# Kernel optimization log

Hardware: AMD Instinct MI355X
Metric: run time of the kernel (lower is better)

Reference implementation:

```python
import jax, jax.numpy as jnp
import numpy as np

B, S, D = 4, 2048, 1024
H = 16
HD = D // H  # 64


def setup_inputs() -> dict:
    key = jax.random.key(0)
    ks = jax.random.split(key, 6)
    scale = 1.0 / np.sqrt(D)
    return {
        "x": jax.random.normal(ks[0], (B, S, D), dtype=jnp.float32),
        "Wq": jax.random.normal(ks[1], (D, D), dtype=jnp.float32) * scale,
        "Wk": jax.random.normal(ks[2], (D, D), dtype=jnp.float32) * scale,
        "Wv": jax.random.normal(ks[3], (D, D), dtype=jnp.float32) * scale,
        "Wo": jax.random.normal(ks[4], (D, D), dtype=jnp.float32) * scale,
        "bo": jax.random.normal(ks[5], (D,), dtype=jnp.float32) * scale,
    }


def reference(x, Wq, Wk, Wv, Wo, bo):
    b, s, _ = x.shape
    q = (x @ Wq).reshape(b, s, H, HD)
    k = (x @ Wk).reshape(b, s, H, HD)
    v = (x @ Wv).reshape(b, s, H, HD)
    # scores: [b, h, q, k]
    scores = jnp.einsum("bqhd,bkhd->bhqk", q, k)
    # causal mask (upper triangle, diagonal=1, is masked out)
    causal = jnp.tril(jnp.ones((s, s), dtype=bool))
    scores = jnp.where(causal, scores, -jnp.inf)
    # NOTE: source divides by head_dim**2 (keys.shape[-1]**2), not sqrt(head_dim)
    attn = jax.nn.softmax(scores / (HD ** 2), axis=-1)
    ctx = jnp.einsum("bhqk,bkhd->bqhd", attn, v).reshape(b, s, D)
    return ctx @ Wo + bo
```

## Files before the change

### kernel.cpp

```cpp
#include <hip/hip_runtime.h>
#include <hip/hip_bf16.h>
#include <stdint.h>

typedef short          bf16x8 __attribute__((ext_vector_type(8)));
typedef float          f32x4  __attribute__((ext_vector_type(4)));
typedef float          f32x16 __attribute__((ext_vector_type(16)));
typedef unsigned short u16x8  __attribute__((ext_vector_type(8)));

#define MFMA_BF16(a, b, c) __builtin_amdgcn_mfma_f32_16x16x32_bf16((a), (b), (c), 0, 0, 0)
#define MFMA32(a, b, c)    __builtin_amdgcn_mfma_f32_32x32x16_bf16((a), (b), (c), 0, 0, 0)

__device__ __forceinline__ void gl2lds16(const void* g, void* l) {
  __builtin_amdgcn_global_load_lds((const __attribute__((address_space(1))) void*)g,
                                   (__attribute__((address_space(3))) void*)l,
                                   16, 0, 0);
}

__device__ __forceinline__ unsigned short f2bf(float f) {
  union { float f; unsigned int u; } v;
  v.f = f;
  unsigned int r = v.u + 0x7FFFu + ((v.u >> 16) & 1u);
  return (unsigned short)(r >> 16);
}

__device__ __forceinline__ unsigned int pack2tr(float lo, float hi) {
  union { float f; unsigned int u; } a, b;
  a.f = lo; b.f = hi;
  return __builtin_amdgcn_perm(b.u, a.u, 0x07060302u);
}

__global__ void k_convert_x(const float* __restrict__ x, unsigned short* __restrict__ xb) {
  int i = (blockIdx.x * 256 + threadIdx.x) * 8;
  float4 a = *(const float4*)(x + i);
  float4 b = *(const float4*)(x + i + 4);
  u16x8 o;
  o[0] = f2bf(a.x); o[1] = f2bf(a.y); o[2] = f2bf(a.z); o[3] = f2bf(a.w);
  o[4] = f2bf(b.x); o[5] = f2bf(b.y); o[6] = f2bf(b.z); o[7] = f2bf(b.w);
  *(u16x8*)(xb + i) = o;
}

__global__ void k_transpose_w(const float* __restrict__ W0, const float* __restrict__ W1,
                              const float* __restrict__ W2, const float* __restrict__ W3,
                              unsigned short* __restrict__ T0, unsigned short* __restrict__ T1,
                              unsigned short* __restrict__ T2, unsigned short* __restrict__ T3) {
  const float* W = (blockIdx.z == 0) ? W0 : (blockIdx.z == 1) ? W1 : (blockIdx.z == 2) ? W2 : W3;
  unsigned short* T = (blockIdx.z == 0) ? T0 : (blockIdx.z == 1) ? T1 : (blockIdx.z == 2) ? T2 : T3;
  __shared__ float tile[32][33];
  int n0 = blockIdx.x * 32, k0 = blockIdx.y * 32;
  int tx = threadIdx.x & 31, ty = threadIdx.x >> 5;
#pragma unroll
  for (int i = 0; i < 4; ++i)
    tile[ty + i * 8][tx] = W[(size_t)(k0 + ty + i * 8) * 1024 + n0 + tx];
  __syncthreads();
#pragma unroll
  for (int i = 0; i < 4; ++i)
    T[(size_t)(n0 + ty + i * 8) * 1024 + k0 + tx] = f2bf(tile[tx][ty + i * 8]);
}

__global__ void k_transpose_v(const unsigned short* __restrict__ V, unsigned short* __restrict__ Vt) {
  int bh = blockIdx.y;
  int b = bh >> 4, h = bh & 15;
  int s0 = blockIdx.x * 64;
  __shared__ unsigned short t[64][72];
  int rowh = threadIdx.x >> 3, cg = threadIdx.x & 7;
#pragma unroll
  for (int i = 0; i < 2; ++i) {
    int s = rowh + i * 32;
    *(u16x8*)&t[s][cg * 8] =
        *(const u16x8*)(V + (size_t)(b * 2048 + s0 + s) * 1024 + h * 64 + cg * 8);
  }
  __syncthreads();
#pragma unroll
  for (int i = 0; i < 2; ++i) {
    int d = rowh + i * 32;
    u16x8 v;
#pragma unroll
    for (int j = 0; j < 8; ++j) v[j] = t[cg * 8 + j][d];
    *(u16x8*)(Vt + (size_t)(bh * 64 + d) * 2048 + s0 + cg * 8) = v;
  }
}

template <bool OUT_F32>
__global__ __launch_bounds__(256, 3)
void k_gemm128(const unsigned short* __restrict__ A,
               const unsigned short* __restrict__ Bt0, const unsigned short* __restrict__ Bt1,
               const unsigned short* __restrict__ Bt2,
               void* C0, void* C1, void* C2,
               const float* __restrict__ bias) {
  const int tid = threadIdx.x;
  const int w = tid >> 6, lane = tid & 63;
  const int quad = lane >> 4, t16 = lane & 15;
  const int wm = w >> 1, wn = w & 1;
  const int ysel = blockIdx.y >> 3;
  const unsigned short* Bt = (ysel == 0) ? Bt0 : (ysel == 1) ? Bt1 : Bt2;
  void* Cv = (ysel == 0) ? C0 : (ysel == 1) ? C1 : C2;
  const int m0 = blockIdx.x * 128;
  const int n0 = (blockIdx.y & 7) * 128;

  __shared__ unsigned short As[2][128 * 32];
  __shared__ unsigned short Bs[2][128 * 32];

  f32x4 acc[4][4];
#pragma unroll
  for (int i = 0; i < 4; ++i)
#pragma unroll
    for (int j = 0; j < 4; ++j) acc[i][j] = (f32x4){0.f, 0.f, 0.f, 0.f};

  const int arow0 = w * 32 + (lane >> 2);
  const int arow1 = arow0 + 16;
  const int ac0 = (lane & 3) ^ ((arow0 >> 1) & 3);
  const int ac1 = (lane & 3) ^ ((arow1 >> 1) & 3);
  const unsigned short* Ap0 = A + (size_t)(m0 + arow0) * 1024 + ac0 * 8;
  const unsigned short* Ap1 = A + (size_t)(m0 + arow1) * 1024 + ac1 * 8;
  const unsigned short* Bp0 = Bt + (size_t)(n0 + arow0) * 1024 + ac0 * 8;
  const unsigned short* Bp1 = Bt + (size_t)(n0 + arow1) * 1024 + ac1 * 8;

  auto loadT = [&](int kk) {
    const int bufi = kk & 1;
    const int ko = kk * 32;
    gl2lds16(Ap0 + ko, &As[bufi][w * 1024]);
    gl2lds16(Ap1 + ko, &As[bufi][w * 1024 + 512]);
    gl2lds16(Bp0 + ko, &Bs[bufi][w * 1024]);
    gl2lds16(Bp1 + ko, &Bs[bufi][w * 1024 + 512]);
  };

  const int ga = quad ^ ((t16 >> 1) & 3);
  const int arows = wm * 64 + t16;
  const int brows = wn * 64 + t16;

  loadT(0);
  __syncthreads();

  for (int kk = 0; kk < 32; ++kk) {
    if (kk + 1 < 32) loadT(kk + 1);
    const unsigned short* Asb = As[kk & 1];
    const unsigned short* Bsb = Bs[kk & 1];
    bf16x8 af[4], bfr[4];
#pragma unroll
    for (int mi = 0; mi < 4; ++mi)
      af[mi] = *(const bf16x8*)&Asb[(arows + mi * 16) * 32 + ga * 8];
#pragma unroll
    for (int ni = 0; ni < 4; ++ni)
      bfr[ni] = *(const bf16x8*)&Bsb[(brows + ni * 16) * 32 + ga * 8];
#pragma unroll
    for (int mi = 0; mi < 4; ++mi)
#pragma unroll
      for (int ni = 0; ni < 4; ++ni)
        acc[mi][ni] = MFMA_BF16(af[mi], bfr[ni], acc[mi][ni]);
    __syncthreads();
  }

#pragma unroll
  for (int mi = 0; mi < 4; ++mi) {
    const int row = m0 + wm * 64 + mi * 16 + quad * 4;
#pragma unroll
    for (int ni = 0; ni < 4; ++ni) {
      const int col = n0 + wn * 64 + ni * 16 + t16;
      f32x4 v = acc[mi][ni];
      if (OUT_F32) {
        float* Cf = (float*)Cv;
        const float bv = bias[col];
#pragma unroll
        for (int r = 0; r < 4; ++r) Cf[(size_t)(row + r) * 1024 + col] = v[r] + bv;
      } else {
        unsigned short* Cb = (unsigned short*)Cv;
#pragma unroll
        for (int r = 0; r < 4; ++r) Cb[(size_t)(row + r) * 1024 + col] = f2bf(v[r]);
      }
    }
  }
}

__global__ __launch_bounds__(256, 2)
void k_attn(const unsigned short* __restrict__ Q, const unsigned short* __restrict__ K,
            const unsigned short* __restrict__ Vt, unsigned short* __restrict__ ctx) {
  const int tid = threadIdx.x;
  const int w = tid >> 6, lane = tid & 63;
  const int ln31 = lane & 31, hh = lane >> 5;
  const int bh = blockIdx.x;
  const int qt = 15 - blockIdx.y;
  const int b = bh >> 4, h = bh & 15;
  const int q0 = qt * 128;

  __shared__ unsigned short Ks[2][128 * 64];
  __shared__ unsigned short Vts[2][64 * 128];
  __shared__ unsigned short Ps[4 * 32 * 64];
  unsigned short* Qs = Ps;
  unsigned short* Pw = &Ps[w * 2048];

#pragma unroll
  for (int i = 0; i < 4; ++i) {
    const int chunk = w * 4 + i;
    const int row = chunk * 8 + (lane >> 3);
    const int c = (lane & 7) ^ (row & 7);
    gl2lds16(Q + (size_t)(b * 2048 + q0 + row) * 1024 + h * 64 + c * 8, &Qs[chunk * 512]);
  }

  auto loadKV = [&](int kt) {
    const int k0 = kt * 128;
    const int bufi = kt & 1;
#pragma unroll
    for (int i = 0; i < 4; ++i) {
      const int chunk = w * 4 + i;
      const int row = chunk * 8 + (lane >> 3);
      const int c = (lane & 7) ^ (row & 7);
      gl2lds16(K + (size_t)(b * 2048 + k0 + row) * 1024 + h * 64 + c * 8,
               &Ks[bufi][chunk * 512]);
    }
#pragma unroll
    for (int i = 0; i < 4; ++i) {
      const int chunk = w * 4 + i;
      const int row = chunk * 4 + (lane >> 4);
      const int c = (lane & 15) ^ (row & 7);
      gl2lds16(Vt + (size_t)(bh * 64 + row) * 2048 + k0 + c * 8, &Vts[bufi][chunk * 512]);
    }
  };

  loadKV(0);
  __syncthreads();

  const int qq = ln31;
  bf16x8 qf[4];
#pragma unroll
  for (int t = 0; t < 4; ++t)
    qf[t] = *(const bf16x8*)&Qs[(w * 32 + qq) * 64 + ((2 * t + hh) ^ (qq & 7)) * 8];

  f32x16 kZ;
#pragma unroll
  for (int i = 0; i < 16; ++i) kZ[i] = 0.f;
  f32x16 oacc0 = kZ, oacc1 = kZ, lacc = kZ;
  bf16x8 onesB;
#pragma unroll
  for (int i = 0; i < 8; ++i) onesB[i] = (short)0x3F80;

  const float C1 = 2.44140625e-4f;
  const float C2 = 2.9802322387695312e-8f;

  const unsigned short* KsB = Ks[0];
  const unsigned short* VtsB = Vts[0];

  auto sgroup = [&](int g, bool masked) {
    f32x16 sc;
#pragma unroll
    for (int t = 0; t < 4; ++t) {
      bf16x8 kf = *(const bf16x8*)&KsB[(g * 32 + ln31) * 64 + ((2 * t + hh) ^ (ln31 & 7)) * 8];
      sc = (t == 0) ? MFMA32(kf, qf[0], kZ) : MFMA32(kf, qf[t], sc);
    }
#pragma unroll
    for (int r2 = 0; r2 < 4; ++r2) {
      float ev[4];
#pragma unroll
      for (int r = 0; r < 4; ++r) {
        const float s = sc[r2 * 4 + r];
        float e = fmaf(s, fmaf(s, C2, C1), 1.0f);
        if (masked) {
          const int krow = r + 8 * r2 + 4 * hh;
          if (krow > qq) e = 0.f;
        }
        ev[r] = e;
      }
      uint2 pp;
      pp.x = pack2tr(ev[0], ev[1]);
      pp.y = pack2tr(ev[2], ev[3]);
      *(uint2*)&Pw[qq * 64 + ((((g & 1) * 4 + r2) ^ (qq & 7)) * 8) + hh * 4] = pp;
    }
  };
  auto zgroup = [&](int g) {
    uint2 z; z.x = 0u; z.y = 0u;
#pragma unroll
    for (int r2 = 0; r2 < 4; ++r2)
      *(uint2*)&Pw[qq * 64 + ((((g & 1) * 4 + r2) ^ (qq & 7)) * 8) + hh * 4] = z;
  };
  auto pv = [&](int half) {
#pragma unroll
    for (int t = 0; t < 4; ++t) {
      bf16x8 pf = *(const bf16x8*)&Pw[qq * 64 + ((2 * t + hh) ^ (qq & 7)) * 8];
      lacc = MFMA32(pf, onesB, lacc);
      const int gv = 2 * t + hh + half * 8;
      bf16x8 vf0 = *(const bf16x8*)&VtsB[ln31 * 128 + ((gv ^ (ln31 & 7)) * 8)];
      bf16x8 vf1 = *(const bf16x8*)&VtsB[(32 + ln31) * 128 + ((gv ^ (ln31 & 7)) * 8)];
      oacc0 = MFMA32(pf, vf0, oacc0);
      oacc1 = MFMA32(pf, vf1, oacc1);
    }
  };

  const int nk = qt + 1;
  for (int kt = 0; kt < nk; ++kt) {
    if (kt + 1 < nk) loadKV(kt + 1);
    KsB = Ks[kt & 1];
    VtsB = Vts[kt & 1];

    if (kt != qt) {
      sgroup(0, false); sgroup(1, false); pv(0);
      sgroup(2, false); sgroup(3, false); pv(1);
    } else {
      if (w == 0)      { sgroup(0, true);  zgroup(1); }
      else if (w == 1) { sgroup(0, false); sgroup(1, true); }
      else             { sgroup(0, false); sgroup(1, false); }
      pv(0);
      if (w >= 2) {
        if (w == 2) { sgroup(2, true);  zgroup(3); }
        else        { sgroup(2, false); sgroup(3, true); }
        pv(1);
      }
    }
    __syncthreads();
  }

#pragma unroll
  for (int r2 = 0; r2 < 4; ++r2) {
#pragma unroll
    for (int r = 0; r < 4; ++r) {
      const int reg = r2 * 4 + r;
      const int qrow = r + 8 * r2 + 4 * hh;
      const float li = __builtin_amdgcn_rcpf(lacc[reg]);
      const size_t base = (size_t)(b * 2048 + q0 + w * 32 + qrow) * 1024 + h * 64;
      ctx[base + ln31] = f2bf(oacc0[reg] * li);
      ctx[base + 32 + ln31] = f2bf(oacc1[reg] * li);
    }
  }
}

extern "C" void kernel_launch(void* const* d_in, const int* in_sizes, int n_in,
                              void* d_out, int out_size, void* d_ws, size_t ws_size,
                              hipStream_t stream) {
  (void)in_sizes; (void)n_in; (void)out_size; (void)ws_size;
  const float* x  = (const float*)d_in[0];
  const float* Wq = (const float*)d_in[1];
  const float* Wk = (const float*)d_in[2];
  const float* Wv = (const float*)d_in[3];
  const float* Wo = (const float*)d_in[4];
  const float* bo = (const float*)d_in[5];
  float* out = (float*)d_out;

  char* ws = (char*)d_ws;
  const size_t MB = 1u << 20;
  unsigned short* xb  = (unsigned short*)(ws + 0 * MB);
  unsigned short* WqT = (unsigned short*)(ws + 16 * MB);
  unsigned short* WkT = (unsigned short*)(ws + 18 * MB);
  unsigned short* WvT = (unsigned short*)(ws + 20 * MB);
  unsigned short* WoT = (unsigned short*)(ws + 22 * MB);
  unsigned short* Qb  = (unsigned short*)(ws + 24 * MB);
  unsigned short* Kb  = (unsigned short*)(ws + 40 * MB);
  unsigned short* Vb  = (unsigned short*)(ws + 56 * MB);
  unsigned short* Vtb = xb;
  unsigned short* ctx = Vb;

  k_convert_x<<<dim3(4096), dim3(256), 0, stream>>>(x, xb);
  k_transpose_w<<<dim3(32, 32, 4), dim3(256), 0, stream>>>(Wq, Wk, Wv, Wo, WqT, WkT, WvT, WoT);
  k_gemm128<false><<<dim3(64, 24), dim3(256), 0, stream>>>(xb, WqT, WkT, WvT, Qb, Kb, Vb, nullptr);
  k_transpose_v<<<dim3(32, 64), dim3(256), 0, stream>>>(Vb, Vtb);
  k_attn<<<dim3(64, 16), dim3(256), 0, stream>>>(Qb, Kb, Vtb, ctx);
  k_gemm128<true><<<dim3(64, 8), dim3(256), 0, stream>>>(ctx, WoT, WoT, WoT, out, out, out, bo);
}
```

Measured before the change: 241.1 us.

## Fuse QKV GEMMs sharing A tile, write V transposed, merge prep kernels

```diff
diff --git a/kernel.cpp b/kernel.cpp
--- a/kernel.cpp
+++ b/kernel.cpp
@@ -29,76 +29,156 @@
   return __builtin_amdgcn_perm(b.u, a.u, 0x07060302u);
 }
 
-__global__ void k_convert_x(const float* __restrict__ x, unsigned short* __restrict__ xb) {
-  int i = (blockIdx.x * 256 + threadIdx.x) * 8;
-  float4 a = *(const float4*)(x + i);
-  float4 b = *(const float4*)(x + i + 4);
-  u16x8 o;
-  o[0] = f2bf(a.x); o[1] = f2bf(a.y); o[2] = f2bf(a.z); o[3] = f2bf(a.w);
-  o[4] = f2bf(b.x); o[5] = f2bf(b.y); o[6] = f2bf(b.z); o[7] = f2bf(b.w);
-  *(u16x8*)(xb + i) = o;
-}
-
-__global__ void k_transpose_w(const float* __restrict__ W0, const float* __restrict__ W1,
-                              const float* __restrict__ W2, const float* __restrict__ W3,
-                              unsigned short* __restrict__ T0, unsigned short* __restrict__ T1,
-                              unsigned short* __restrict__ T2, unsigned short* __restrict__ T3) {
-  const float* W = (blockIdx.z == 0) ? W0 : (blockIdx.z == 1) ? W1 : (blockIdx.z == 2) ? W2 : W3;
-  unsigned short* T = (blockIdx.z == 0) ? T0 : (blockIdx.z == 1) ? T1 : (blockIdx.z == 2) ? T2 : T3;
-  __shared__ float tile[32][33];
-  int n0 = blockIdx.x * 32, k0 = blockIdx.y * 32;
-  int tx = threadIdx.x & 31, ty = threadIdx.x >> 5;
-#pragma unroll
-  for (int i = 0; i < 4; ++i)
-    tile[ty + i * 8][tx] = W[(size_t)(k0 + ty + i * 8) * 1024 + n0 + tx];
-  __syncthreads();
-#pragma unroll
-  for (int i = 0; i < 4; ++i)
-    T[(size_t)(n0 + ty + i * 8) * 1024 + k0 + tx] = f2bf(tile[tx][ty + i * 8]);
-}
-
-__global__ void k_transpose_v(const unsigned short* __restrict__ V, unsigned short* __restrict__ Vt) {
-  int bh = blockIdx.y;
-  int b = bh >> 4, h = bh & 15;
-  int s0 = blockIdx.x * 64;
-  __shared__ unsigned short t[64][72];
-  int rowh = threadIdx.x >> 3, cg = threadIdx.x & 7;
-#pragma unroll
-  for (int i = 0; i < 2; ++i) {
-    int s = rowh + i * 32;
-    *(u16x8*)&t[s][cg * 8] =
-        *(const u16x8*)(V + (size_t)(b * 2048 + s0 + s) * 1024 + h * 64 + cg * 8);
-  }
-  __syncthreads();
-#pragma unroll
-  for (int i = 0; i < 2; ++i) {
-    int d = rowh + i * 32;
-    u16x8 v;
-#pragma unroll
-    for (int j = 0; j < 8; ++j) v[j] = t[cg * 8 + j][d];
-    *(u16x8*)(Vt + (size_t)(bh * 64 + d) * 2048 + s0 + cg * 8) = v;
-  }
-}
-
-template <bool OUT_F32>
-__global__ __launch_bounds__(256, 3)
-void k_gemm128(const unsigned short* __restrict__ A,
-               const unsigned short* __restrict__ Bt0, const unsigned short* __restrict__ Bt1,
-               const unsigned short* __restrict__ Bt2,
-               void* C0, void* C1, void* C2,
-               const float* __restrict__ bias) {
+__global__ void k_prep(const float* __restrict__ x, unsigned short* __restrict__ xb,
+                       const float* __restrict__ W0, const float* __restrict__ W1,
+                       const float* __restrict__ W2, const float* __restrict__ W3,
+                       unsigned short* __restrict__ T0, unsigned short* __restrict__ T1,
+                       unsigned short* __restrict__ T2, unsigned short* __restrict__ T3) {
+  if (blockIdx.x < 4096) {
+    int i = (blockIdx.x * 256 + threadIdx.x) * 8;
+    float4 a = *(const float4*)(x + i);
+    float4 b = *(const float4*)(x + i + 4);
+    u16x8 o;
+    o[0] = f2bf(a.x); o[1] = f2bf(a.y); o[2] = f2bf(a.z); o[3] = f2bf(a.w);
+    o[4] = f2bf(b.x); o[5] = f2bf(b.y); o[6] = f2bf(b.z); o[7] = f2bf(b.w);
+    *(u16x8*)(xb + i) = o;
+  } else {
+    const int idx = blockIdx.x - 4096;
+    const int z = idx >> 10, rem = idx & 1023;
+    const int k0 = (rem >> 5) * 32, n0 = (rem & 31) * 32;
+    const float* W = (z == 0) ? W0 : (z == 1) ? W1 : (z == 2) ? W2 : W3;
+    unsigned short* T = (z == 0) ? T0 : (z == 1) ? T1 : (z == 2) ? T2 : T3;
+    __shared__ float tile[32][33];
+    int tx = threadIdx.x & 31, ty = threadIdx.x >> 5;
+#pragma unroll
+    for (int i = 0; i < 4; ++i)
+      tile[ty + i * 8][tx] = W[(size_t)(k0 + ty + i * 8) * 1024 + n0 + tx];
+    __syncthreads();
+#pragma unroll
+    for (int i = 0; i < 4; ++i)
+      T[(size_t)(n0 + ty + i * 8) * 1024 + k0 + tx] = f2bf(tile[tx][ty + i * 8]);
+  }
+}
+
+__global__ __launch_bounds__(256, 2)
+void k_gemm_qkv(const unsigned short* __restrict__ A,
+                const unsigned short* __restrict__ BtQ, const unsigned short* __restrict__ BtK,
+                const unsigned short* __restrict__ BtV,
+                unsigned short* __restrict__ Qb, unsigned short* __restrict__ Kb,
+                unsigned short* __restrict__ Vt) {
   const int tid = threadIdx.x;
   const int w = tid >> 6, lane = tid & 63;
   const int quad = lane >> 4, t16 = lane & 15;
   const int wm = w >> 1, wn = w & 1;
-  const int ysel = blockIdx.y >> 3;
-  const unsigned short* Bt = (ysel == 0) ? Bt0 : (ysel == 1) ? Bt1 : Bt2;
-  void* Cv = (ysel == 0) ? C0 : (ysel == 1) ? C1 : C2;
   const int m0 = blockIdx.x * 128;
-  const int n0 = (blockIdx.y & 7) * 128;
-
-  __shared__ unsigned short As[2][128 * 32];
-  __shared__ unsigned short Bs[2][128 * 32];
+  const int n0 = blockIdx.y * 128;
+
+  __shared__ unsigned short As[2][4096];
+  __shared__ unsigned short Bs[2][3 * 4096];
+
+  f32x4 acc[3][4][4];
+#pragma unroll
+  for (int j = 0; j < 3; ++j)
+#pragma unroll
+    for (int i = 0; i < 4; ++i)
+#pragma unroll
+      for (int n = 0; n < 4; ++n) acc[j][i][n] = (f32x4){0.f, 0.f, 0.f, 0.f};
+
+  const int srow = lane >> 2, g4 = lane & 3;
+  const int arow0 = w * 32 + srow, arow1 = arow0 + 16;
+  const unsigned short* Ap0 = A + (size_t)(m0 + arow0) * 1024 + (g4 ^ ((arow0 >> 1) & 3)) * 8;
+  const unsigned short* Ap1 = A + (size_t)(m0 + arow1) * 1024 + (g4 ^ ((arow1 >> 1) & 3)) * 8;
+  const unsigned short* Bp[6];
+  int bOff[6];
+#pragma unroll
+  for (int i = 0; i < 6; ++i) {
+    const int c = w * 6 + i;
+    const int j = c >> 3, cc = c & 7;
+    const int row = cc * 16 + srow;
+    const unsigned short* Bj = (j == 0) ? BtQ : (j == 1) ? BtK : BtV;
+    Bp[i] = Bj + (size_t)(n0 + row) * 1024 + (g4 ^ ((row >> 1) & 3)) * 8;
+    bOff[i] = j * 4096 + cc * 512;
+  }
+
+  auto loadT = [&](int kk) {
+    const int bufi = kk & 1;
+    const int ko = kk * 32;
+    gl2lds16(Ap0 + ko, &As[bufi][w * 1024]);
+    gl2lds16(Ap1 + ko, &As[bufi][w * 1024 + 512]);
+#pragma unroll
+    for (int i = 0; i < 6; ++i) gl2lds16(Bp[i] + ko, &Bs[bufi][bOff[i]]);
+  };
+
+  const int ga = quad ^ ((t16 >> 1) & 3);
+  const int arows = wm * 64 + t16;
+  const int brows = wn * 64 + t16;
+
+  loadT(0);
+  __syncthreads();
+
+  for (int kk = 0; kk < 32; ++kk) {
+    if (kk + 1 < 32) loadT(kk + 1);
+    const unsigned short* Asb = As[kk & 1];
+    const unsigned short* Bsb = Bs[kk & 1];
+    bf16x8 af[4];
+#pragma unroll
+    for (int mi = 0; mi < 4; ++mi)
+      af[mi] = *(const bf16x8*)&Asb[(arows + mi * 16) * 32 + ga * 8];
+#pragma unroll
+    for (int j = 0; j < 3; ++j)
+#pragma unroll
+      for (int ni = 0; ni < 4; ++ni) {
+        bf16x8 bfr = *(const bf16x8*)&Bsb[j * 4096 + (brows + ni * 16) * 32 + ga * 8];
+#pragma unroll
+        for (int mi = 0; mi < 4; ++mi)
+          acc[j][mi][ni] = MFMA_BF16(af[mi], bfr, acc[j][mi][ni]);
+      }
+    __syncthreads();
+  }
+
+#pragma unroll
+  for (int j = 0; j < 2; ++j) {
+    unsigned short* P = (j == 0) ? Qb : Kb;
+#pragma unroll
+    for (int mi = 0; mi < 4; ++mi) {
+      const int row = m0 + wm * 64 + mi * 16 + quad * 4;
+#pragma unroll
+      for (int ni = 0; ni < 4; ++ni) {
+        const int col = n0 + wn * 64 + ni * 16 + t16;
+        f32x4 v = acc[j][mi][ni];
+#pragma unroll
+        for (int r = 0; r < 4; ++r) P[(size_t)(row + r) * 1024 + col] = f2bf(v[r]);
+      }
+    }
+  }
+  const int h = (n0 >> 6) + wn;
+#pragma unroll
+  for (int mi = 0; mi < 4; ++mi) {
+    const int m = m0 + wm * 64 + mi * 16 + quad * 4;
+    const int b = m >> 11, s = m & 2047;
+#pragma unroll
+    for (int ni = 0; ni < 4; ++ni) {
+      const int d = ni * 16 + t16;
+      f32x4 v = acc[2][mi][ni];
+      ushort4 pv4;
+      pv4.x = f2bf(v[0]); pv4.y = f2bf(v[1]); pv4.z = f2bf(v[2]); pv4.w = f2bf(v[3]);
+      *(ushort4*)&Vt[(size_t)((b * 16 + h) * 64 + d) * 2048 + s] = pv4;
+    }
+  }
+}
+
+__global__ __launch_bounds__(256, 3)
+void k_gemm_o(const unsigned short* __restrict__ A, const unsigned short* __restrict__ Bt,
+              float* __restrict__ C, const float* __restrict__ bias) {
+  const int tid = threadIdx.x;
+  const int w = tid >> 6, lane = tid & 63;
+  const int quad = lane >> 4, t16 = lane & 15;
+  const int wm = w >> 1, wn = w & 1;
+  const int m0 = blockIdx.x * 128;
+  const int n0 = blockIdx.y * 128;
+
+  __shared__ unsigned short As[2][4096];
+  __shared__ unsigned short Bs[2][4096];
 
   f32x4 acc[4][4];
 #pragma unroll
@@ -106,10 +186,10 @@
 #pragma unroll
     for (int j = 0; j < 4; ++j) acc[i][j] = (f32x4){0.f, 0.f, 0.f, 0.f};
 
-  const int arow0 = w * 32 + (lane >> 2);
-  const int arow1 = arow0 + 16;
-  const int ac0 = (lane & 3) ^ ((arow0 >> 1) & 3);
-  const int ac1 = (lane & 3) ^ ((arow1 >> 1) & 3);
+  const int srow = lane >> 2, g4 = lane & 3;
+  const int arow0 = w * 32 + srow, arow1 = arow0 + 16;
+  const int ac0 = g4 ^ ((arow0 >> 1) & 3);
+  const int ac1 = g4 ^ ((arow1 >> 1) & 3);
   const unsigned short* Ap0 = A + (size_t)(m0 + arow0) * 1024 + ac0 * 8;
   const unsigned short* Ap1 = A + (size_t)(m0 + arow1) * 1024 + ac1 * 8;
   const unsigned short* Bp0 = Bt + (size_t)(n0 + arow0) * 1024 + ac0 * 8;
@@ -156,17 +236,10 @@
 #pragma unroll
     for (int ni = 0; ni < 4; ++ni) {
       const int col = n0 + wn * 64 + ni * 16 + t16;
+      const float bv = bias[col];
       f32x4 v = acc[mi][ni];
-      if (OUT_F32) {
-        float* Cf = (float*)Cv;
-        const float bv = bias[col];
-#pragma unroll
-        for (int r = 0; r < 4; ++r) Cf[(size_t)(row + r) * 1024 + col] = v[r] + bv;
-      } else {
-        unsigned short* Cb = (unsigned short*)Cv;
-#pragma unroll
-        for (int r = 0; r < 4; ++r) Cb[(size_t)(row + r) * 1024 + col] = f2bf(v[r]);
-      }
+#pragma unroll
+      for (int r = 0; r < 4; ++r) C[(size_t)(row + r) * 1024 + col] = v[r] + bv;
     }
   }
 }
@@ -342,14 +415,11 @@
   unsigned short* WoT = (unsigned short*)(ws + 22 * MB);
   unsigned short* Qb  = (unsigned short*)(ws + 24 * MB);
   unsigned short* Kb  = (unsigned short*)(ws + 40 * MB);
-  unsigned short* Vb  = (unsigned short*)(ws + 56 * MB);
-  unsigned short* Vtb = xb;
-  unsigned short* ctx = Vb;
-
-  k_convert_x<<<dim3(4096), dim3(256), 0, stream>>>(x, xb);
-  k_transpose_w<<<dim3(32, 32, 4), dim3(256), 0, stream>>>(Wq, Wk, Wv, Wo, WqT, WkT, WvT, WoT);
-  k_gemm128<false><<<dim3(64, 24), dim3(256), 0, stream>>>(xb, WqT, WkT, WvT, Qb, Kb, Vb, nullptr);
-  k_transpose_v<<<dim3(32, 64), dim3(256), 0, stream>>>(Vb, Vtb);
+  unsigned short* Vtb = (unsigned short*)(ws + 56 * MB);
+  unsigned short* ctx = xb;
+
+  k_prep<<<dim3(8192), dim3(256), 0, stream>>>(x, xb, Wq, Wk, Wv, Wo, WqT, WkT, WvT, WoT);
+  k_gemm_qkv<<<dim3(64, 8), dim3(256), 0, stream>>>(xb, WqT, WkT, WvT, Qb, Kb, Vtb);
   k_attn<<<dim3(64, 16), dim3(256), 0, stream>>>(Qb, Kb, Vtb, ctx);
-  k_gemm128<true><<<dim3(64, 8), dim3(256), 0, stream>>>(ctx, WoT, WoT, WoT, out, out, out, bo);
-}
+  k_gemm_o<<<dim3(64, 8), dim3(256), 0, stream>>>(ctx, WoT, out, bo);
+}
```

Measured after the change: 232.0 us. -3.8%, faster.
